# Kernel tuning notes

Hardware: AMD Instinct MI355X
Metric: run time of the kernel (lower is better)

The kernel has to match this reference:

```python
import math
import jax, jax.numpy as jnp
import numpy as np

N_HEADS = 16

def setup_inputs() -> dict:
    key = jax.random.key(0)
    k1, k2, k3 = jax.random.split(key, 3)
    B, T, C = 2, 2048, 1024
    x = jax.random.normal(k1, (B, T, C), dtype=jnp.float32)
    # Linear weights stored as [in, out] so y = x @ W + b (same math as torch Linear)
    w_qkv = jax.random.normal(k2, (C, 3 * C), dtype=jnp.float32) * (1.0 / math.sqrt(C))
    b_qkv = jnp.zeros((3 * C,), dtype=jnp.float32)
    w_out = jax.random.normal(k3, (C, C), dtype=jnp.float32) * (1.0 / math.sqrt(C))
    b_out = jnp.zeros((C,), dtype=jnp.float32)
    return {"x": x, "w_qkv": w_qkv, "b_qkv": b_qkv, "w_out": w_out, "b_out": b_out}

def reference(x, w_qkv, b_qkv, w_out, b_out):
    B, T, C = x.shape
    H = N_HEADS
    hd = C // H
    qkv = (x @ w_qkv + b_qkv).reshape(B, T, 3, H, hd)
    q, k, v = qkv[:, :, 0], qkv[:, :, 1], qkv[:, :, 2]  # [B,T,H,hd]
    scale = 1.0 / math.sqrt(hd)
    att = jnp.einsum('bqhd,bkhd->bhqk', q, k) * scale  # [B,H,T,T]
    causal = jnp.tril(jnp.ones((T, T), dtype=bool))
    att = jnp.where(causal[None, None], att, jnp.float32(-jnp.inf))
    att = jax.nn.softmax(att, axis=-1)
    # dropout p=0.0 -> identity (eval mode)
    y = jnp.einsum('bhqk,bkhd->bqhd', att, v).reshape(B, T, C)
    return y @ w_out + b_out
```

## Files before the change

kernel.cpp:

```cpp
#include <hip/hip_runtime.h>
#include <hip/hip_bf16.h>
#include <stdint.h>


typedef __bf16 bf16_t;
typedef __attribute__((ext_vector_type(8))) __bf16 bf16x8;
typedef __attribute__((ext_vector_type(4))) __bf16 bf16x4;
typedef __attribute__((ext_vector_type(4))) short short4v;
typedef __attribute__((ext_vector_type(4))) float f32x4;

static_assert(sizeof(bf16x8) == 16, "bf16x8 must be 16B");

#if defined(__has_builtin)
#if __has_builtin(__builtin_amdgcn_exp2f)
#define EXP2F(x) __builtin_amdgcn_exp2f(x)
#endif
#endif
#ifndef EXP2F
#define EXP2F(x) exp2f(x)
#endif

__device__ inline void async_copy16(const bf16_t* gsrc, bf16_t* lds_dst) {
  __builtin_amdgcn_global_load_lds(
      (const __attribute__((address_space(1))) uint32_t*)(const void*)gsrc,
      (__attribute__((address_space(3))) uint32_t*)(void*)lds_dst,
      16, 0, 0);
}

__global__ __launch_bounds__(256) void prep_kernel(
    const float* __restrict__ x, const float* __restrict__ wq,
    const float* __restrict__ wo, bf16_t* __restrict__ xb,
    bf16_t* __restrict__ wqkvT, bf16_t* __restrict__ woutT) {
  __shared__ bf16_t tile[32][33];
  const int bid = blockIdx.x;
  if (bid < 2048) {
    const int i = bid * 256 + threadIdx.x;
    const float4* s = (const float4*)x;
    float4 a = s[i * 2], b = s[i * 2 + 1];
    bf16x8 o;
    o[0] = (bf16_t)a.x; o[1] = (bf16_t)a.y; o[2] = (bf16_t)a.z; o[3] = (bf16_t)a.w;
    o[4] = (bf16_t)b.x; o[5] = (bf16_t)b.y; o[6] = (bf16_t)b.z; o[7] = (bf16_t)b.w;
    ((bf16x8*)xb)[i] = o;
    return;
  }
  const bool isq = bid < 5120;
  const int id = isq ? bid - 2048 : bid - 5120;
  const int C = isq ? 3072 : 1024;
  const int R = 1024;
  const int nbx = isq ? 96 : 32;
  const float* in = isq ? wq : wo;
  bf16_t* out = isq ? wqkvT : woutT;
  const int c0 = (id % nbx) * 32, r0 = (id / nbx) * 32;
  const int tx4 = threadIdx.x & 7;
  const int ty = threadIdx.x >> 3;
  {
    const float4 ld =
        *(const float4*)&in[(size_t)(r0 + ty) * C + c0 + tx4 * 4];
    tile[ty][tx4 * 4 + 0] = (bf16_t)ld.x;
    tile[ty][tx4 * 4 + 1] = (bf16_t)ld.y;
    tile[ty][tx4 * 4 + 2] = (bf16_t)ld.z;
    tile[ty][tx4 * 4 + 3] = (bf16_t)ld.w;
  }
  __syncthreads();
  {
    bf16x4 w;
    w[0] = tile[tx4 * 4 + 0][ty];
    w[1] = tile[tx4 * 4 + 1][ty];
    w[2] = tile[tx4 * 4 + 2][ty];
    w[3] = tile[tx4 * 4 + 3][ty];
    *(bf16x4*)&out[(size_t)(c0 + ty) * R + r0 + tx4 * 4] = w;
  }
}

template <bool OUT_F32>
__global__ __launch_bounds__(256, 3) void gemm_bt_kernel(
    const bf16_t* __restrict__ A, const bf16_t* __restrict__ Bt,
    const float* __restrict__ bias, void* __restrict__ Cv, int M, int N,
    int K) {
  __shared__ __align__(16) bf16_t sA[128 * 64];
  __shared__ __align__(16) bf16_t sB[128 * 64];
  const int tid = threadIdx.x;
  const int wave = tid >> 6, lane = tid & 63;
  const int quad = lane >> 4, l16 = lane & 15;
  const int wm = (wave >> 1) * 64, wn = (wave & 1) * 64;
  const int bm = blockIdx.y * 128, bn = blockIdx.x * 128;

  const int rl = lane >> 3, cl = lane & 7;
  const int srow = wave * 32;
  const bf16_t* gA =
      A + (size_t)(bm + srow + rl) * K + (size_t)((cl ^ rl) << 3);
  const bf16_t* gB =
      Bt + (size_t)(bn + srow + rl) * K + (size_t)((cl ^ rl) << 3);
  bf16_t* lA = sA + srow * 64;
  bf16_t* lB = sB + srow * 64;

  f32x4 acc[4][4] = {};

  for (int k0 = 0; k0 < K; k0 += 64) {
    __syncthreads();
#pragma unroll
    for (int c = 0; c < 4; c++) {
      async_copy16(gA + (size_t)(c * 8) * K + k0, lA + c * 512);
      async_copy16(gB + (size_t)(c * 8) * K + k0, lB + c * 512);
    }
    __syncthreads();

#pragma unroll
    for (int h = 0; h < 2; h++) {
      bf16x8 af[4], bfr[4];
#pragma unroll
      for (int i = 0; i < 4; i++) {
        const int row = wm + i * 16 + l16;
        af[i] = *(const bf16x8*)&sA[row * 64 +
                                    (((h * 4 + quad) ^ (row & 7)) << 3)];
      }
#pragma unroll
      for (int j = 0; j < 4; j++) {
        const int row = wn + j * 16 + l16;
        bfr[j] = *(const bf16x8*)&sB[row * 64 +
                                     (((h * 4 + quad) ^ (row & 7)) << 3)];
      }
#pragma unroll
      for (int i = 0; i < 4; i++)
#pragma unroll
        for (int j = 0; j < 4; j++)
          acc[i][j] = __builtin_amdgcn_mfma_f32_16x16x32_bf16(
              af[i], bfr[j], acc[i][j], 0, 0, 0);
    }
  }

#pragma unroll
  for (int j = 0; j < 4; j++) {
    const int col = bn + wn + j * 16 + l16;
    const float bv = bias[col];
#pragma unroll
    for (int i = 0; i < 4; i++) {
#pragma unroll
      for (int r = 0; r < 4; r++) {
        const int row = bm + wm + i * 16 + quad * 4 + r;
        const float v = acc[i][j][r] + bv;
        if (OUT_F32)
          ((float*)Cv)[(size_t)row * N + col] = v;
        else
          ((bf16_t*)Cv)[(size_t)row * N + col] = (bf16_t)v;
      }
    }
  }
}

__global__ __launch_bounds__(256) void gemm_bt64_kernel(
    const bf16_t* __restrict__ A, const bf16_t* __restrict__ Bt,
    const float* __restrict__ bias, float* __restrict__ C, int M, int N,
    int K) {
  __shared__ __align__(16) bf16_t sA[64 * 64];
  __shared__ __align__(16) bf16_t sB[128 * 64];
  const int tid = threadIdx.x;
  const int wave = tid >> 6, lane = tid & 63;
  const int quad = lane >> 4, l16 = lane & 15;
  const int wm = (wave >> 1) * 32, wn = (wave & 1) * 64;
  const int bm = blockIdx.y * 64, bn = blockIdx.x * 128;

  const int rl = lane >> 3, cl = lane & 7;
  const bf16_t* gA =
      A + (size_t)(bm + wave * 16 + rl) * K + (size_t)((cl ^ rl) << 3);
  bf16_t* lA = sA + (wave * 16) * 64;
  const bf16_t* gB =
      Bt + (size_t)(bn + wave * 32 + rl) * K + (size_t)((cl ^ rl) << 3);
  bf16_t* lB = sB + (wave * 32) * 64;

  f32x4 acc[2][4] = {};

  for (int k0 = 0; k0 < K; k0 += 64) {
    __syncthreads();
#pragma unroll
    for (int c = 0; c < 2; c++)
      async_copy16(gA + (size_t)(c * 8) * K + k0, lA + c * 512);
#pragma unroll
    for (int c = 0; c < 4; c++)
      async_copy16(gB + (size_t)(c * 8) * K + k0, lB + c * 512);
    __syncthreads();

#pragma unroll
    for (int h = 0; h < 2; h++) {
      bf16x8 af[2], bfr[4];
#pragma unroll
      for (int i = 0; i < 2; i++) {
        const int row = wm + i * 16 + l16;
        af[i] = *(const bf16x8*)&sA[row * 64 +
                                    (((h * 4 + quad) ^ (row & 7)) << 3)];
      }
#pragma unroll
      for (int j = 0; j < 4; j++) {
        const int row = wn + j * 16 + l16;
        bfr[j] = *(const bf16x8*)&sB[row * 64 +
                                     (((h * 4 + quad) ^ (row & 7)) << 3)];
      }
#pragma unroll
      for (int i = 0; i < 2; i++)
#pragma unroll
        for (int j = 0; j < 4; j++)
          acc[i][j] = __builtin_amdgcn_mfma_f32_16x16x32_bf16(
              af[i], bfr[j], acc[i][j], 0, 0, 0);
    }
  }

#pragma unroll
  for (int j = 0; j < 4; j++) {
    const int col = bn + wn + j * 16 + l16;
    const float bv = bias[col];
#pragma unroll
    for (int i = 0; i < 2; i++) {
#pragma unroll
      for (int r = 0; r < 4; r++) {
        const int row = bm + wm + i * 16 + quad * 4 + r;
        C[(size_t)row * N + col] = acc[i][j][r] + bv;
      }
    }
  }
}

__global__ __launch_bounds__(512, 4) void attn_kernel(
    const bf16_t* __restrict__ qkv, bf16_t* __restrict__ Y) {
  constexpr int T = 2048, C3 = 3072;
  constexpr float CSC = 0.18033688f;
  constexpr float MB = 20.0f;
  __shared__ __align__(16) bf16_t sK[2][64 * 64];
  __shared__ __align__(16) bf16_t sVt[2][64 * 64];

  const int tid = threadIdx.x;
  const int wave = tid >> 6, lane = tid & 63;
  const int quad = lane >> 4, l16 = lane & 15;
  const int wq = wave >> 1;
  const int jh = wave & 1;
  const int bh = blockIdx.y;
  const int flip = (bh >> 3) & 1;
  const int vv = ((int)blockIdx.x + ((bh >> 4) & 1) * 8) & 31;
  const int X = flip ? (31 - vv) : vv;
  const int q0 = X * 64;
  const int b = bh >> 4, h = bh & 15;
  const size_t base = (size_t)b * T * C3 + (size_t)h * 64;

  const int qrow = q0 + wq * 16 + l16;
  const bf16x8 qf0 = *(const bf16x8*)&qkv[base + (size_t)qrow * C3 + quad * 8];
  const bf16x8 qf1 =
      *(const bf16x8*)&qkv[base + (size_t)qrow * C3 + 32 + quad * 8];

  f32x4 o[4] = {};
  f32x4 l4 = {0.f, 0.f, 0.f, 0.f};

  const bool krole = tid < 256;
  const int st = (tid & 255) >> 2, sseg = tid & 3;
  const bf16_t* gK = &qkv[base + (size_t)st * C3 + 1024 + sseg * 16];
  const int kq = (tid & 255) >> 4, dq = tid & 15;
  const bf16_t* gV = &qkv[base + (size_t)(4 * kq) * C3 + 2048 + dq * 4];

  bf16x8 kr0 = {}, kr1 = {};
  bf16x4 vA0 = {}, vA1 = {}, vA2 = {}, vA3 = {};
  if (krole) {
    kr0 = *(const bf16x8*)gK;
    kr1 = *(const bf16x8*)(gK + 8);
  } else {
    vA0 = *(const bf16x4*)gV;
    vA1 = *(const bf16x4*)(gV + C3);
    vA2 = *(const bf16x4*)(gV + 2 * C3);
    vA3 = *(const bf16x4*)(gV + 3 * C3);
  }

  for (int kt = 0; kt < X; kt++) {
    const int p = kt & 1;
    if (krole) {
      *(bf16x8*)&sK[p][st * 64 + (((2 * sseg + 0) ^ (st & 7)) << 3)] = kr0;
      *(bf16x8*)&sK[p][st * 64 + (((2 * sseg + 1) ^ (st & 7)) << 3)] = kr1;
    } else {
#pragma unroll
      for (int i = 0; i < 4; i++) {
        const int d = dq * 4 + i;
        bf16x4 w;
        w[0] = vA0[i]; w[1] = vA1[i]; w[2] = vA2[i]; w[3] = vA3[i];
        *(bf16x4*)&sVt[p][d * 64 + ((kq ^ (d & 15)) << 2)] = w;
      }
    }
    {
      const size_t off = (size_t)(kt + 1) * 64 * C3;
      if (krole) {
        kr0 = *(const bf16x8*)(gK + off);
        kr1 = *(const bf16x8*)(gK + off + 8);
      } else {
        vA0 = *(const bf16x4*)(gV + off);
        vA1 = *(const bf16x4*)(gV + off + C3);
        vA2 = *(const bf16x4*)(gV + off + 2 * C3);
        vA3 = *(const bf16x4*)(gV + off + 3 * C3);
      }
    }
    __syncthreads();

#pragma unroll
    for (int jj = 0; jj < 2; jj++) {
      const int j = jh * 2 + jj;
      const int trow = j * 16 + l16;
      bf16x8 kf0 =
          *(const bf16x8*)&sK[p][trow * 64 + ((quad ^ (trow & 7)) << 3)];
      bf16x8 kf1 =
          *(const bf16x8*)&sK[p][trow * 64 + (((4 + quad) ^ (trow & 7)) << 3)];
      f32x4 s2 = {};
      __builtin_amdgcn_s_setprio(1);
      s2 = __builtin_amdgcn_mfma_f32_16x16x32_bf16(kf0, qf0, s2, 0, 0, 0);
      s2 = __builtin_amdgcn_mfma_f32_16x16x32_bf16(kf1, qf1, s2, 0, 0, 0);
      __builtin_amdgcn_s_setprio(0);
#pragma unroll
      for (int r = 0; r < 4; r++) s2[r] = EXP2F(fmaf(s2[r], CSC, -MB));
      l4 += s2;
      bf16x4 pb;
      pb[0] = (bf16_t)s2[0]; pb[1] = (bf16_t)s2[1];
      pb[2] = (bf16_t)s2[2]; pb[3] = (bf16_t)s2[3];
      union { bf16x4 bv; short4v sv; } u;
      u.bv = pb;
      const short4v pa = u.sv;
      __builtin_amdgcn_s_setprio(1);
#pragma unroll
      for (int n16 = 0; n16 < 4; n16++) {
        const int d = n16 * 16 + l16;
        const short4v vf = *(const short4v*)&sVt[p][d * 64 +
                                                    (((j * 4 + quad) ^ (d & 15))
                                                     << 2)];
        o[n16] =
            __builtin_amdgcn_mfma_f32_16x16x16bf16_1k(pa, vf, o[n16], 0, 0, 0);
      }
      __builtin_amdgcn_s_setprio(0);
    }
  }

  {
    const int p = X & 1;
    if (krole) {
      *(bf16x8*)&sK[p][st * 64 + (((2 * sseg + 0) ^ (st & 7)) << 3)] = kr0;
      *(bf16x8*)&sK[p][st * 64 + (((2 * sseg + 1) ^ (st & 7)) << 3)] = kr1;
    } else {
#pragma unroll
      for (int i = 0; i < 4; i++) {
        const int d = dq * 4 + i;
        bf16x4 w;
        w[0] = vA0[i]; w[1] = vA1[i]; w[2] = vA2[i]; w[3] = vA3[i];
        *(bf16x4*)&sVt[p][d * 64 + ((kq ^ (d & 15)) << 2)] = w;
      }
    }
    __syncthreads();

#pragma unroll
    for (int jj = 0; jj < 2; jj++) {
      const int j = jh * 2 + jj;
      if (j > wq) continue;
      const int trow = j * 16 + l16;
      bf16x8 kf0 =
          *(const bf16x8*)&sK[p][trow * 64 + ((quad ^ (trow & 7)) << 3)];
      bf16x8 kf1 =
          *(const bf16x8*)&sK[p][trow * 64 + (((4 + quad) ^ (trow & 7)) << 3)];
      f32x4 s2 = {};
      __builtin_amdgcn_s_setprio(1);
      s2 = __builtin_amdgcn_mfma_f32_16x16x32_bf16(kf0, qf0, s2, 0, 0, 0);
      s2 = __builtin_amdgcn_mfma_f32_16x16x32_bf16(kf1, qf1, s2, 0, 0, 0);
      __builtin_amdgcn_s_setprio(0);
      const bool diag = (j == wq);
#pragma unroll
      for (int r = 0; r < 4; r++) {
        float pv = EXP2F(fmaf(s2[r], CSC, -MB));
        if (diag && (quad * 4 + r > l16)) pv = 0.f;
        s2[r] = pv;
      }
      l4 += s2;
      bf16x4 pb;
      pb[0] = (bf16_t)s2[0]; pb[1] = (bf16_t)s2[1];
      pb[2] = (bf16_t)s2[2]; pb[3] = (bf16_t)s2[3];
      union { bf16x4 bv; short4v sv; } u;
      u.bv = pb;
      const short4v pa = u.sv;
      __builtin_amdgcn_s_setprio(1);
#pragma unroll
      for (int n16 = 0; n16 < 4; n16++) {
        const int d = n16 * 16 + l16;
        const short4v vf = *(const short4v*)&sVt[p][d * 64 +
                                                    (((j * 4 + quad) ^ (d & 15))
                                                     << 2)];
        o[n16] =
            __builtin_amdgcn_mfma_f32_16x16x16bf16_1k(pa, vf, o[n16], 0, 0, 0);
      }
      __builtin_amdgcn_s_setprio(0);
    }
  }

  float l_acc = (l4[0] + l4[1]) + (l4[2] + l4[3]);
  l_acc += __shfl_xor(l_acc, 16);
  l_acc += __shfl_xor(l_acc, 32);

  __syncthreads();
  float* mo = (float*)&sK[0][0];
  float* ml = (float*)&sVt[0][0];
  if (jh == 1) {
    float* dst = mo + ((size_t)(wq * 64 + lane)) * 16;
#pragma unroll
    for (int n16 = 0; n16 < 4; n16++) *(f32x4*)(dst + n16 * 4) = o[n16];
    if (quad == 0) ml[wq * 16 + l16] = l_acc;
  }
  __syncthreads();
  if (jh == 0) {
    const float* src = mo + ((size_t)(wq * 64 + lane)) * 16;
#pragma unroll
    for (int n16 = 0; n16 < 4; n16++) o[n16] += *(const f32x4*)(src + n16 * 4);
    const float lsum = l_acc + ml[wq * 16 + l16];
#pragma unroll
    for (int r = 0; r < 4; r++) {
      const float lr = __shfl(lsum, quad * 4 + r);
      const float inv = 1.0f / lr;
      const int row = q0 + wq * 16 + quad * 4 + r;
#pragma unroll
      for (int n16 = 0; n16 < 4; n16++)
        Y[((size_t)b * T + row) * 1024 + h * 64 + n16 * 16 + l16] =
            (bf16_t)(o[n16][r] * inv);
    }
  }
}

extern "C" void kernel_launch(void* const* d_in, const int* in_sizes, int n_in,
                              void* d_out, int out_size, void* d_ws,
                              size_t ws_size, hipStream_t stream) {
  const float* x = nullptr;
  const float* w_qkv = nullptr;
  const float* b_qkv = nullptr;
  const float* w_out = nullptr;
  const float* b_out = nullptr;
  for (int i = 0; i < n_in; i++) {
    switch (in_sizes[i]) {
      case 4194304: x = (const float*)d_in[i]; break;
      case 3145728: w_qkv = (const float*)d_in[i]; break;
      case 3072:    b_qkv = (const float*)d_in[i]; break;
      case 1048576: w_out = (const float*)d_in[i]; break;
      case 1024:    b_out = (const float*)d_in[i]; break;
      default: break;
    }
  }
  float* out = (float*)d_out;

  bf16_t* xb = (bf16_t*)d_ws;
  bf16_t* wqkvT = xb + (size_t)4194304;
  bf16_t* woutT = wqkvT + (size_t)3145728;
  bf16_t* qkv = woutT + (size_t)1048576;
  bf16_t* Y = qkv + (size_t)12582912;

  prep_kernel<<<6144, 256, 0, stream>>>(x, w_qkv, w_out, xb, wqkvT, woutT);
  gemm_bt_kernel<false><<<dim3(24, 32), 256, 0, stream>>>(
      xb, wqkvT, b_qkv, (void*)qkv, 4096, 3072, 1024);
  attn_kernel<<<dim3(32, 32), 512, 0, stream>>>(qkv, Y);
  gemm_bt64_kernel<<<dim3(8, 64), 256, 0, stream>>>(
      Y, woutT, b_out, out, 4096, 1024, 1024);
}
```

Measured before the change: 196.0 us.

## Use 256-thread attention blocks with async K loads direct to LDS

The attention kernel drops from 8 waves to 4 waves per block. Each wave now owns 16 query rows and loops over all four 16-key sub-tiles, which removes the cross-wave split of keys and the LDS reduction of partial O and l at the end. K tiles are now prefetched with global_load_lds async copies straight into the double-buffered shared memory, using an XOR swizzle on the source address. V keeps the register-staged transpose. The changes cut thread count, the final reduction and its barriers, and register staging for K. In exchange each wave does twice the MFMA work per tile, and correctness depends on the async copy landing before the next barrier without an explicit wait.

```diff
diff --git a/kernel.cpp b/kernel.cpp
--- a/kernel.cpp
+++ b/kernel.cpp
@@ -219,7 +219,7 @@
   }
 }
 
-__global__ __launch_bounds__(512, 4) void attn_kernel(
+__global__ __launch_bounds__(256, 4) void attn_kernel(
     const bf16_t* __restrict__ qkv, bf16_t* __restrict__ Y) {
   constexpr int T = 2048, C3 = 3072;
   constexpr float CSC = 0.18033688f;
@@ -230,8 +230,6 @@
   const int tid = threadIdx.x;
   const int wave = tid >> 6, lane = tid & 63;
   const int quad = lane >> 4, l16 = lane & 15;
-  const int wq = wave >> 1;
-  const int jh = wave & 1;
   const int bh = blockIdx.y;
   const int flip = (bh >> 3) & 1;
   const int vv = ((int)blockIdx.x + ((bh >> 4) & 1) * 8) & 31;
@@ -240,7 +238,7 @@
   const int b = bh >> 4, h = bh & 15;
   const size_t base = (size_t)b * T * C3 + (size_t)h * 64;
 
-  const int qrow = q0 + wq * 16 + l16;
+  const int qrow = q0 + wave * 16 + l16;
   const bf16x8 qf0 = *(const bf16x8*)&qkv[base + (size_t)qrow * C3 + quad * 8];
   const bf16x8 qf1 =
       *(const bf16x8*)&qkv[base + (size_t)qrow * C3 + 32 + quad * 8];
@@ -248,55 +246,49 @@
   f32x4 o[4] = {};
   f32x4 l4 = {0.f, 0.f, 0.f, 0.f};
 
-  const bool krole = tid < 256;
-  const int st = (tid & 255) >> 2, sseg = tid & 3;
-  const bf16_t* gK = &qkv[base + (size_t)st * C3 + 1024 + sseg * 16];
-  const int kq = (tid & 255) >> 4, dq = tid & 15;
+  const int krr = lane >> 3, kcc = lane & 7;
+  const bf16_t* gKa =
+      &qkv[base + (size_t)(16 * wave + krr) * C3 + 1024 + ((kcc ^ krr) << 3)];
+  bf16_t* const lK0 = (bf16_t*)&sK[0][(16 * wave) * 64];
+  bf16_t* const lK1 = (bf16_t*)&sK[1][(16 * wave) * 64];
+
+  const int kq = tid >> 4, dq = tid & 15;
   const bf16_t* gV = &qkv[base + (size_t)(4 * kq) * C3 + 2048 + dq * 4];
 
-  bf16x8 kr0 = {}, kr1 = {};
-  bf16x4 vA0 = {}, vA1 = {}, vA2 = {}, vA3 = {};
-  if (krole) {
-    kr0 = *(const bf16x8*)gK;
-    kr1 = *(const bf16x8*)(gK + 8);
-  } else {
-    vA0 = *(const bf16x4*)gV;
-    vA1 = *(const bf16x4*)(gV + C3);
-    vA2 = *(const bf16x4*)(gV + 2 * C3);
-    vA3 = *(const bf16x4*)(gV + 3 * C3);
-  }
+  async_copy16(gKa, lK0);
+  async_copy16(gKa + (size_t)8 * C3, lK0 + 8 * 64);
+  bf16x4 vA0 = *(const bf16x4*)gV;
+  bf16x4 vA1 = *(const bf16x4*)(gV + C3);
+  bf16x4 vA2 = *(const bf16x4*)(gV + 2 * C3);
+  bf16x4 vA3 = *(const bf16x4*)(gV + 3 * C3);
 
   for (int kt = 0; kt < X; kt++) {
     const int p = kt & 1;
-    if (krole) {
-      *(bf16x8*)&sK[p][st * 64 + (((2 * sseg + 0) ^ (st & 7)) << 3)] = kr0;
-      *(bf16x8*)&sK[p][st * 64 + (((2 * sseg + 1) ^ (st & 7)) << 3)] = kr1;
-    } else {
-#pragma unroll
-      for (int i = 0; i < 4; i++) {
-        const int d = dq * 4 + i;
-        bf16x4 w;
-        w[0] = vA0[i]; w[1] = vA1[i]; w[2] = vA2[i]; w[3] = vA3[i];
-        *(bf16x4*)&sVt[p][d * 64 + ((kq ^ (d & 15)) << 2)] = w;
-      }
+#pragma unroll
+    for (int i = 0; i < 4; i++) {
+      const int d = dq * 4 + i;
+      bf16x4 w;
+      w[0] = vA0[i]; w[1] = vA1[i]; w[2] = vA2[i]; w[3] = vA3[i];
+      *(bf16x4*)&sVt[p][d * 64 + ((kq ^ (d & 15)) << 2)] = w;
     }
     {
       const size_t off = (size_t)(kt + 1) * 64 * C3;
-      if (krole) {
-        kr0 = *(const bf16x8*)(gK + off);
-        kr1 = *(const bf16x8*)(gK + off + 8);
-      } else {
-        vA0 = *(const bf16x4*)(gV + off);
-        vA1 = *(const bf16x4*)(gV + off + C3);
-        vA2 = *(const bf16x4*)(gV + off + 2 * C3);
-        vA3 = *(const bf16x4*)(gV + off + 3 * C3);
-      }
-    }
-    __syncthreads();
-
-#pragma unroll
-    for (int jj = 0; jj < 2; jj++) {
-      const int j = jh * 2 + jj;
+      vA0 = *(const bf16x4*)(gV + off);
+      vA1 = *(const bf16x4*)(gV + off + C3);
+      vA2 = *(const bf16x4*)(gV + off + 2 * C3);
+      vA3 = *(const bf16x4*)(gV + off + 3 * C3);
+    }
+    __syncthreads();
+
+    {
+      const size_t off = (size_t)(kt + 1) * 64 * C3;
+      bf16_t* const lKn = p ? lK0 : lK1;
+      async_copy16(gKa + off, lKn);
+      async_copy16(gKa + off + (size_t)8 * C3, lKn + 8 * 64);
+    }
+
+#pragma unroll
+    for (int j = 0; j < 4; j++) {
       const int trow = j * 16 + l16;
       bf16x8 kf0 =
           *(const bf16x8*)&sK[p][trow * 64 + ((quad ^ (trow & 7)) << 3)];
@@ -332,24 +324,18 @@
 
   {
     const int p = X & 1;
-    if (krole) {
-      *(bf16x8*)&sK[p][st * 64 + (((2 * sseg + 0) ^ (st & 7)) << 3)] = kr0;
-      *(bf16x8*)&sK[p][st * 64 + (((2 * sseg + 1) ^ (st & 7)) << 3)] = kr1;
-    } else {
-#pragma unroll
-      for (int i = 0; i < 4; i++) {
-        const int d = dq * 4 + i;
-        bf16x4 w;
-        w[0] = vA0[i]; w[1] = vA1[i]; w[2] = vA2[i]; w[3] = vA3[i];
-        *(bf16x4*)&sVt[p][d * 64 + ((kq ^ (d & 15)) << 2)] = w;
-      }
-    }
-    __syncthreads();
-
-#pragma unroll
-    for (int jj = 0; jj < 2; jj++) {
-      const int j = jh * 2 + jj;
-      if (j > wq) continue;
+#pragma unroll
+    for (int i = 0; i < 4; i++) {
+      const int d = dq * 4 + i;
+      bf16x4 w;
+      w[0] = vA0[i]; w[1] = vA1[i]; w[2] = vA2[i]; w[3] = vA3[i];
+      *(bf16x4*)&sVt[p][d * 64 + ((kq ^ (d & 15)) << 2)] = w;
+    }
+    __syncthreads();
+
+#pragma unroll
+    for (int j = 0; j < 4; j++) {
+      if (j > wave) continue;
       const int trow = j * 16 + l16;
       bf16x8 kf0 =
           *(const bf16x8*)&sK[p][trow * 64 + ((quad ^ (trow & 7)) << 3)];
@@ -360,7 +346,7 @@
       s2 = __builtin_amdgcn_mfma_f32_16x16x32_bf16(kf0, qf0, s2, 0, 0, 0);
       s2 = __builtin_amdgcn_mfma_f32_16x16x32_bf16(kf1, qf1, s2, 0, 0, 0);
       __builtin_amdgcn_s_setprio(0);
-      const bool diag = (j == wq);
+      const bool diag = (j == wave);
 #pragma unroll
       for (int r = 0; r < 4; r++) {
         float pv = EXP2F(fmaf(s2[r], CSC, -MB));
@@ -391,32 +377,15 @@
   float l_acc = (l4[0] + l4[1]) + (l4[2] + l4[3]);
   l_acc += __shfl_xor(l_acc, 16);
   l_acc += __shfl_xor(l_acc, 32);
-
-  __syncthreads();
-  float* mo = (float*)&sK[0][0];
-  float* ml = (float*)&sVt[0][0];
-  if (jh == 1) {
-    float* dst = mo + ((size_t)(wq * 64 + lane)) * 16;
-#pragma unroll
-    for (int n16 = 0; n16 < 4; n16++) *(f32x4*)(dst + n16 * 4) = o[n16];
-    if (quad == 0) ml[wq * 16 + l16] = l_acc;
-  }
-  __syncthreads();
-  if (jh == 0) {
-    const float* src = mo + ((size_t)(wq * 64 + lane)) * 16;
-#pragma unroll
-    for (int n16 = 0; n16 < 4; n16++) o[n16] += *(const f32x4*)(src + n16 * 4);
-    const float lsum = l_acc + ml[wq * 16 + l16];
-#pragma unroll
-    for (int r = 0; r < 4; r++) {
-      const float lr = __shfl(lsum, quad * 4 + r);
-      const float inv = 1.0f / lr;
-      const int row = q0 + wq * 16 + quad * 4 + r;
-#pragma unroll
-      for (int n16 = 0; n16 < 4; n16++)
-        Y[((size_t)b * T + row) * 1024 + h * 64 + n16 * 16 + l16] =
-            (bf16_t)(o[n16][r] * inv);
-    }
+#pragma unroll
+  for (int r = 0; r < 4; r++) {
+    const float lr = __shfl(l_acc, quad * 4 + r);
+    const float inv = 1.0f / lr;
+    const int row = q0 + wave * 16 + quad * 4 + r;
+#pragma unroll
+    for (int n16 = 0; n16 < 4; n16++)
+      Y[((size_t)b * T + row) * 1024 + h * 64 + n16 * 16 + l16] =
+          (bf16_t)(o[n16][r] * inv);
   }
 }
 
@@ -449,7 +418,7 @@
   prep_kernel<<<6144, 256, 0, stream>>>(x, w_qkv, w_out, xb, wqkvT, woutT);
   gemm_bt_kernel<false><<<dim3(24, 32), 256, 0, stream>>>(
       xb, wqkvT, b_qkv, (void*)qkv, 4096, 3072, 1024);
-  attn_kernel<<<dim3(32, 32), 512, 0, stream>>>(qkv, Y);
+  attn_kernel<<<dim3(32, 32), 256, 0, stream>>>(qkv, Y);
   gemm_bt64_kernel<<<dim3(8, 64), 256, 0, stream>>>(
       Y, woutT, b_out, out, 4096, 1024, 1024);
 }
```

Result: faster. 173.1 us (-11.7%).
